# Kernel tuning notes

Hardware: AMD Instinct MI355X
Metric: run time of the kernel (lower is better)

The kernel has to match this reference:

```python
import jax, jax.numpy as jnp
import numpy as np

B, N, F, U, NH = 1, 4096, 32, 32, 2
NEG = -1e10


def _leaky(x):
    # tf.nn.leaky_relu default alpha = 0.2
    return jnp.where(x >= 0, x, 0.2 * x)


def setup_inputs() -> dict:
    key = jax.random.key(0)
    k = jax.random.split(key, 6)
    H_r = jax.random.normal(k[0], (B, N, F), dtype=jnp.float32)
    H_i = jax.random.normal(k[1], (B, N, F), dtype=jnp.float32)
    # sparse-ish adjacency with self loops, stored dense as the module expects
    adj = (jax.random.uniform(k[2], (B, N, N)) < 0.005).astype(jnp.float32)
    A = jnp.maximum(adj, jnp.eye(N, dtype=jnp.float32)[None])
    s_w = float(np.sqrt(6.0 / (F + U)))
    s_a = float(np.sqrt(6.0 / (U + 1)))
    W = jax.random.uniform(k[3], (NH, F, U), minval=-s_w, maxval=s_w, dtype=jnp.float32)
    a1 = jax.random.uniform(k[4], (NH, U), minval=-s_a, maxval=s_a, dtype=jnp.float32)
    a2 = jax.random.uniform(k[5], (NH, U), minval=-s_a, maxval=s_a, dtype=jnp.float32)
    return {"H_r": H_r, "H_i": H_i, "A": A, "W": W, "a1": a1, "a2": a2}


def reference(H_r, H_i, A, W, a1, a2):
    # complex X = H @ W  (W real): decompose into real/imag, vectorized over heads
    Xr = jnp.einsum('bnf,hfu->hbnu', H_r, W)   # [NH,B,N,U]
    Xi = jnp.einsum('bnf,hfu->hbnu', H_i, W)
    # additive attention logits: self + neighbours^T
    sr = jnp.einsum('hbnu,hu->hbn', Xr, a1)
    si = jnp.einsum('hbnu,hu->hbn', Xi, a1)
    nr = jnp.einsum('hbnu,hu->hbn', Xr, a2)
    ni = jnp.einsum('hbnu,hu->hbn', Xi, a2)
    E1 = _leaky(sr[..., :, None] + nr[..., None, :])   # [NH,B,N,N]
    E2 = _leaky(si[..., :, None] + ni[..., None, :])
    mask = NEG * (1.0 - A)                              # [B,N,N], broadcasts over heads
    alpha1 = jax.nn.softmax(E1 + mask, axis=-1)
    alpha2 = jax.nn.softmax(E2 + mask, axis=-1)
    # complex alpha @ complex X
    Hr_cap = jnp.einsum('hbij,hbju->hbiu', alpha1, Xr) - jnp.einsum('hbij,hbju->hbiu', alpha2, Xi)
    Hi_cap = jnp.einsum('hbij,hbju->hbiu', alpha1, Xi) + jnp.einsum('hbij,hbju->hbiu', alpha2, Xr)
    # concat heads on feature dim (output_layer=False, activation=identity)
    out_r = jnp.transpose(Hr_cap, (1, 2, 0, 3)).reshape(B, N, NH * U)
    out_i = jnp.transpose(Hi_cap, (1, 2, 0, 3)).reshape(B, N, NH * U)
    return (out_r, out_i)
```

## Files before the change

### kernel.cpp

```cpp
#include <hip/hip_runtime.h>
#include <math.h>

namespace {
constexpr int N  = 4096;
constexpr int F  = 32;
constexpr int U  = 32;
constexpr int NH = 2;
constexpr int MAXNBR = 1024;

__device__ __forceinline__ float leaky(float x) {
    return x >= 0.f ? x : 0.2f * x;
}

__device__ __forceinline__ float wred_max(float v) {
    #pragma unroll
    for (int m = 32; m; m >>= 1) v = fmaxf(v, __shfl_xor(v, m, 64));
    return v;
}
__device__ __forceinline__ float wred_sum(float v) {
    #pragma unroll
    for (int m = 32; m; m >>= 1) v += __shfl_xor(v, m, 64);
    return v;
}

__global__ __launch_bounds__(256) void proj_kernel(
    const float* __restrict__ Hr, const float* __restrict__ Hi,
    const float* __restrict__ W,  const float* __restrict__ a1,
    const float* __restrict__ a2,
    float* __restrict__ Xr, float* __restrict__ Xi,
    float* __restrict__ sr, float* __restrict__ si,
    float* __restrict__ nr, float* __restrict__ ni)
{
    __shared__ float sW[NH * F * U];
    __shared__ float sH[2][8][F];
    const int t = threadIdx.x;
    for (int k = t; k < NH * F * U; k += 256) sW[k] = W[k];
    const int row0 = blockIdx.x * 8;
    {
        const int r = t >> 5, f = t & 31;
        sH[0][r][f] = Hr[(row0 + r) * F + f];
        sH[1][r][f] = Hi[(row0 + r) * F + f];
    }
    __syncthreads();

    const int r = t >> 5, u = t & 31;
    const int n = row0 + r;
    float xr[NH] = {0.f, 0.f}, xi[NH] = {0.f, 0.f};
    #pragma unroll
    for (int h = 0; h < NH; ++h) {
        #pragma unroll
        for (int f = 0; f < F; ++f) {
            const float w = sW[h * F * U + f * U + u];
            xr[h] += sH[0][r][f] * w;
            xi[h] += sH[1][r][f] * w;
        }
    }
    #pragma unroll
    for (int h = 0; h < NH; ++h) {
        Xr[(h * N + n) * U + u] = xr[h];
        Xi[(h * N + n) * U + u] = xi[h];
    }
    #pragma unroll
    for (int h = 0; h < NH; ++h) {
        const float av1 = a1[h * U + u], av2 = a2[h * U + u];
        float vsr = xr[h] * av1, vnr = xr[h] * av2;
        float vsi = xi[h] * av1, vni = xi[h] * av2;
        #pragma unroll
        for (int m = 16; m; m >>= 1) {
            vsr += __shfl_xor(vsr, m, 32);
            vnr += __shfl_xor(vnr, m, 32);
            vsi += __shfl_xor(vsi, m, 32);
            vni += __shfl_xor(vni, m, 32);
        }
        if (u == 0) {
            sr[h * N + n] = vsr;
            nr[h * N + n] = vnr;
            si[h * N + n] = vsi;
            ni[h * N + n] = vni;
        }
    }
}

__global__ __launch_bounds__(256) void attn_kernel(
    const float* __restrict__ A,
    const float* __restrict__ Xr, const float* __restrict__ Xi,
    const float* __restrict__ sr, const float* __restrict__ si,
    const float* __restrict__ nr, const float* __restrict__ ni,
    float* __restrict__ out)
{
    __shared__ int   s_nbr[MAXNBR];
    __shared__ float s_e[4][MAXNBR];
    __shared__ float s_pmax[4][4];
    __shared__ float s_psum[4][4];
    __shared__ float s_accr[256];
    __shared__ float s_acci[256];
    __shared__ int   s_cnt;

    const int i = blockIdx.x;
    const int t = threadIdx.x;
    const int lane = t & 63, wv = t >> 6;

    if (t == 0) s_cnt = 0;
    __syncthreads();

    const float4* Arow = (const float4*)(A + (size_t)i * N);
    #pragma unroll
    for (int k = t; k < N / 4; k += 256) {
        const float4 v = Arow[k];
        if (v.x != 0.f) { int p = atomicAdd(&s_cnt, 1); if (p < MAXNBR) s_nbr[p] = 4 * k + 0; }
        if (v.y != 0.f) { int p = atomicAdd(&s_cnt, 1); if (p < MAXNBR) s_nbr[p] = 4 * k + 1; }
        if (v.z != 0.f) { int p = atomicAdd(&s_cnt, 1); if (p < MAXNBR) s_nbr[p] = 4 * k + 2; }
        if (v.w != 0.f) { int p = atomicAdd(&s_cnt, 1); if (p < MAXNBR) s_nbr[p] = 4 * k + 3; }
    }
    __syncthreads();
    const int cnt = min(s_cnt, MAXNBR);

    float sri[NH], sii[NH];
    #pragma unroll
    for (int h = 0; h < NH; ++h) { sri[h] = sr[h * N + i]; sii[h] = si[h * N + i]; }

    float m[4] = {-INFINITY, -INFINITY, -INFINITY, -INFINITY};
    for (int j = t; j < cnt; j += 256) {
        const int nj = s_nbr[j];
        #pragma unroll
        for (int h = 0; h < NH; ++h) {
            const float e1 = leaky(sri[h] + nr[h * N + nj]);
            const float e2 = leaky(sii[h] + ni[h * N + nj]);
            s_e[2 * h + 0][j] = e1;
            s_e[2 * h + 1][j] = e2;
            m[2 * h + 0] = fmaxf(m[2 * h + 0], e1);
            m[2 * h + 1] = fmaxf(m[2 * h + 1], e2);
        }
    }
    #pragma unroll
    for (int v = 0; v < 4; ++v) {
        const float wm = wred_max(m[v]);
        if (lane == 0) s_pmax[wv][v] = wm;
    }
    __syncthreads();
    float mx[4], sum[4];
    #pragma unroll
    for (int v = 0; v < 4; ++v) {
        mx[v] = fmaxf(fmaxf(s_pmax[0][v], s_pmax[1][v]),
                      fmaxf(s_pmax[2][v], s_pmax[3][v]));
        sum[v] = 0.f;
    }

    for (int j = t; j < cnt; j += 256) {
        #pragma unroll
        for (int v = 0; v < 4; ++v) {
            const float w = __expf(s_e[v][j] - mx[v]);
            s_e[v][j] = w;
            sum[v] += w;
        }
    }
    #pragma unroll
    for (int v = 0; v < 4; ++v) {
        const float ws = wred_sum(sum[v]);
        if (lane == 0) s_psum[wv][v] = ws;
    }
    __syncthreads();
    float rinv[4];
    #pragma unroll
    for (int v = 0; v < 4; ++v)
        rinv[v] = 1.f / (s_psum[0][v] + s_psum[1][v] + s_psum[2][v] + s_psum[3][v]);

    const int g = t >> 6, h = (t >> 5) & 1, u = t & 31;
    const float r1 = rinv[2 * h + 0], r2 = rinv[2 * h + 1];
    float accr = 0.f, acci = 0.f;
    for (int j = g; j < cnt; j += 4) {
        const int nj = s_nbr[j];
        const float w1 = s_e[2 * h + 0][j] * r1;
        const float w2 = s_e[2 * h + 1][j] * r2;
        const float xr = Xr[(h * N + nj) * U + u];
        const float xi = Xi[(h * N + nj) * U + u];
        accr += w1 * xr - w2 * xi;
        acci += w1 * xi + w2 * xr;
    }
    s_accr[t] = accr;
    s_acci[t] = acci;
    __syncthreads();
    if (g == 0) {
        const float vr = s_accr[t] + s_accr[t + 64] + s_accr[t + 128] + s_accr[t + 192];
        const float vi = s_acci[t] + s_acci[t + 64] + s_acci[t + 128] + s_acci[t + 192];
        out[(size_t)i * (NH * U) + h * U + u] = vr;
        out[(size_t)N * NH * U + (size_t)i * (NH * U) + h * U + u] = vi;
    }
}
}

extern "C" void kernel_launch(void* const* d_in, const int* in_sizes, int n_in,
                              void* d_out, int out_size, void* d_ws, size_t ws_size,
                              hipStream_t stream) {
    (void)in_sizes; (void)n_in; (void)out_size; (void)ws_size;
    const float* Hr = (const float*)d_in[0];
    const float* Hi = (const float*)d_in[1];
    const float* A  = (const float*)d_in[2];
    const float* W  = (const float*)d_in[3];
    const float* a1 = (const float*)d_in[4];
    const float* a2 = (const float*)d_in[5];
    float* out = (float*)d_out;

    float* ws = (float*)d_ws;
    float* Xr = ws;
    float* Xi = Xr + NH * N * U;
    float* sr = Xi + NH * N * U;
    float* si = sr + NH * N;
    float* nr = si + NH * N;
    float* ni = nr + NH * N;

    proj_kernel<<<N / 8, 256, 0, stream>>>(Hr, Hi, W, a1, a2, Xr, Xi, sr, si, nr, ni);
    attn_kernel<<<N, 256, 0, stream>>>(A, Xr, Xi, sr, si, nr, ni, out);
}
```

Baseline: 120.5 us.

## Use one wave per row with ballot scan and online softmax

The attention kernel now gives each row to a single wavefront instead of a 256-thread block. Neighbours are found with wave ballots over the adjacency row (with a one-step prefetch) rather than shared-memory atomics. Softmax and aggregation are fused into a single online-softmax pass, and real/imag projections are interleaved as float2 so each neighbour needs one load. This removes the block barriers, shared buffers and the neighbour cap, at the cost of extra exp calls per neighbour and a serial per-neighbour dependency chain inside each wave.

```diff
diff --git a/kernel.cpp b/kernel.cpp
--- a/kernel.cpp
+++ b/kernel.cpp
@@ -6,30 +6,16 @@
 constexpr int F  = 32;
 constexpr int U  = 32;
 constexpr int NH = 2;
-constexpr int MAXNBR = 1024;
 
 __device__ __forceinline__ float leaky(float x) {
     return x >= 0.f ? x : 0.2f * x;
-}
-
-__device__ __forceinline__ float wred_max(float v) {
-    #pragma unroll
-    for (int m = 32; m; m >>= 1) v = fmaxf(v, __shfl_xor(v, m, 64));
-    return v;
-}
-__device__ __forceinline__ float wred_sum(float v) {
-    #pragma unroll
-    for (int m = 32; m; m >>= 1) v += __shfl_xor(v, m, 64);
-    return v;
 }
 
 __global__ __launch_bounds__(256) void proj_kernel(
     const float* __restrict__ Hr, const float* __restrict__ Hi,
     const float* __restrict__ W,  const float* __restrict__ a1,
     const float* __restrict__ a2,
-    float* __restrict__ Xr, float* __restrict__ Xi,
-    float* __restrict__ sr, float* __restrict__ si,
-    float* __restrict__ nr, float* __restrict__ ni)
+    float2* __restrict__ Xp, float2* __restrict__ Sp, float2* __restrict__ Np)
 {
     __shared__ float sW[NH * F * U];
     __shared__ float sH[2][8][F];
@@ -56,10 +42,9 @@
         }
     }
     #pragma unroll
-    for (int h = 0; h < NH; ++h) {
-        Xr[(h * N + n) * U + u] = xr[h];
-        Xi[(h * N + n) * U + u] = xi[h];
-    }
+    for (int h = 0; h < NH; ++h)
+        Xp[(h * N + n) * U + u] = make_float2(xr[h], xi[h]);
+
     #pragma unroll
     for (int h = 0; h < NH; ++h) {
         const float av1 = a1[h * U + u], av2 = a2[h * U + u];
@@ -73,119 +58,70 @@
             vni += __shfl_xor(vni, m, 32);
         }
         if (u == 0) {
-            sr[h * N + n] = vsr;
-            nr[h * N + n] = vnr;
-            si[h * N + n] = vsi;
-            ni[h * N + n] = vni;
+            Sp[h * N + n] = make_float2(vsr, vsi);
+            Np[h * N + n] = make_float2(vnr, vni);
         }
     }
 }
 
 __global__ __launch_bounds__(256) void attn_kernel(
     const float* __restrict__ A,
-    const float* __restrict__ Xr, const float* __restrict__ Xi,
-    const float* __restrict__ sr, const float* __restrict__ si,
-    const float* __restrict__ nr, const float* __restrict__ ni,
+    const float2* __restrict__ Xp, const float2* __restrict__ Sp,
+    const float2* __restrict__ Np,
     float* __restrict__ out)
 {
-    __shared__ int   s_nbr[MAXNBR];
-    __shared__ float s_e[4][MAXNBR];
-    __shared__ float s_pmax[4][4];
-    __shared__ float s_psum[4][4];
-    __shared__ float s_accr[256];
-    __shared__ float s_acci[256];
-    __shared__ int   s_cnt;
+    const int wv   = threadIdx.x >> 6;
+    const int lane = threadIdx.x & 63;
+    const int i    = blockIdx.x * 4 + wv;
+    const int h    = lane >> 5;
 
-    const int i = blockIdx.x;
-    const int t = threadIdx.x;
-    const int lane = t & 63, wv = t >> 6;
+    const float2 s = Sp[h * N + i];
 
-    if (t == 0) s_cnt = 0;
-    __syncthreads();
+    float m1 = -INFINITY, m2 = -INFINITY;
+    float l1 = 0.f, l2 = 0.f;
+    float a1r = 0.f, a1i = 0.f, a2r = 0.f, a2i = 0.f;
 
-    const float4* Arow = (const float4*)(A + (size_t)i * N);
-    #pragma unroll
-    for (int k = t; k < N / 4; k += 256) {
-        const float4 v = Arow[k];
-        if (v.x != 0.f) { int p = atomicAdd(&s_cnt, 1); if (p < MAXNBR) s_nbr[p] = 4 * k + 0; }
-        if (v.y != 0.f) { int p = atomicAdd(&s_cnt, 1); if (p < MAXNBR) s_nbr[p] = 4 * k + 1; }
-        if (v.z != 0.f) { int p = atomicAdd(&s_cnt, 1); if (p < MAXNBR) s_nbr[p] = 4 * k + 2; }
-        if (v.w != 0.f) { int p = atomicAdd(&s_cnt, 1); if (p < MAXNBR) s_nbr[p] = 4 * k + 3; }
+    const float4* __restrict__ Arow = (const float4*)(A + (size_t)i * N);
+    float4 v = Arow[lane];
+    #pragma unroll 1
+    for (int c = 0; c < N / 256; ++c) {
+        float4 vn;
+        if (c < N / 256 - 1) vn = Arow[(c + 1) * 64 + lane];
+        unsigned long long mk0 = __ballot(v.x != 0.f);
+        unsigned long long mk1 = __ballot(v.y != 0.f);
+        unsigned long long mk2 = __ballot(v.z != 0.f);
+        unsigned long long mk3 = __ballot(v.w != 0.f);
+        #pragma unroll
+        for (int cc = 0; cc < 4; ++cc) {
+            unsigned long long mask = (cc == 0) ? mk0 : (cc == 1) ? mk1
+                                    : (cc == 2) ? mk2 : mk3;
+            while (mask) {
+                const int b = __ffsll((unsigned long long)mask) - 1;
+                mask &= mask - 1;
+                const int nj = c * 256 + 4 * b + cc;
+                const float2 nn = Np[h * N + nj];
+                const float e1 = leaky(s.x + nn.x);
+                const float e2 = leaky(s.y + nn.y);
+                const float m1n = fmaxf(m1, e1), m2n = fmaxf(m2, e2);
+                const float c1 = __expf(m1 - m1n);
+                const float c2 = __expf(m2 - m2n);
+                const float w1 = __expf(e1 - m1n);
+                const float w2 = __expf(e2 - m2n);
+                m1 = m1n; m2 = m2n;
+                l1 = l1 * c1 + w1;
+                l2 = l2 * c2 + w2;
+                const float2 x = Xp[(h * N + nj) * U + (lane & 31)];
+                a1r = a1r * c1 + w1 * x.x;
+                a1i = a1i * c1 + w1 * x.y;
+                a2r = a2r * c2 + w2 * x.x;
+                a2i = a2i * c2 + w2 * x.y;
+            }
+        }
+        v = vn;
     }
-    __syncthreads();
-    const int cnt = min(s_cnt, MAXNBR);
-
-    float sri[NH], sii[NH];
-    #pragma unroll
-    for (int h = 0; h < NH; ++h) { sri[h] = sr[h * N + i]; sii[h] = si[h * N + i]; }
-
-    float m[4] = {-INFINITY, -INFINITY, -INFINITY, -INFINITY};
-    for (int j = t; j < cnt; j += 256) {
-        const int nj = s_nbr[j];
-        #pragma unroll
-        for (int h = 0; h < NH; ++h) {
-            const float e1 = leaky(sri[h] + nr[h * N + nj]);
-            const float e2 = leaky(sii[h] + ni[h * N + nj]);
-            s_e[2 * h + 0][j] = e1;
-            s_e[2 * h + 1][j] = e2;
-            m[2 * h + 0] = fmaxf(m[2 * h + 0], e1);
-            m[2 * h + 1] = fmaxf(m[2 * h + 1], e2);
-        }
-    }
-    #pragma unroll
-    for (int v = 0; v < 4; ++v) {
-        const float wm = wred_max(m[v]);
-        if (lane == 0) s_pmax[wv][v] = wm;
-    }
-    __syncthreads();
-    float mx[4], sum[4];
-    #pragma unroll
-    for (int v = 0; v < 4; ++v) {
-        mx[v] = fmaxf(fmaxf(s_pmax[0][v], s_pmax[1][v]),
-                      fmaxf(s_pmax[2][v], s_pmax[3][v]));
-        sum[v] = 0.f;
-    }
-
-    for (int j = t; j < cnt; j += 256) {
-        #pragma unroll
-        for (int v = 0; v < 4; ++v) {
-            const float w = __expf(s_e[v][j] - mx[v]);
-            s_e[v][j] = w;
-            sum[v] += w;
-        }
-    }
-    #pragma unroll
-    for (int v = 0; v < 4; ++v) {
-        const float ws = wred_sum(sum[v]);
-        if (lane == 0) s_psum[wv][v] = ws;
-    }
-    __syncthreads();
-    float rinv[4];
-    #pragma unroll
-    for (int v = 0; v < 4; ++v)
-        rinv[v] = 1.f / (s_psum[0][v] + s_psum[1][v] + s_psum[2][v] + s_psum[3][v]);
-
-    const int g = t >> 6, h = (t >> 5) & 1, u = t & 31;
-    const float r1 = rinv[2 * h + 0], r2 = rinv[2 * h + 1];
-    float accr = 0.f, acci = 0.f;
-    for (int j = g; j < cnt; j += 4) {
-        const int nj = s_nbr[j];
-        const float w1 = s_e[2 * h + 0][j] * r1;
-        const float w2 = s_e[2 * h + 1][j] * r2;
-        const float xr = Xr[(h * N + nj) * U + u];
-        const float xi = Xi[(h * N + nj) * U + u];
-        accr += w1 * xr - w2 * xi;
-        acci += w1 * xi + w2 * xr;
-    }
-    s_accr[t] = accr;
-    s_acci[t] = acci;
-    __syncthreads();
-    if (g == 0) {
-        const float vr = s_accr[t] + s_accr[t + 64] + s_accr[t + 128] + s_accr[t + 192];
-        const float vi = s_acci[t] + s_acci[t + 64] + s_acci[t + 128] + s_acci[t + 192];
-        out[(size_t)i * (NH * U) + h * U + u] = vr;
-        out[(size_t)N * NH * U + (size_t)i * (NH * U) + h * U + u] = vi;
-    }
+    const float r1 = 1.f / l1, r2 = 1.f / l2;
+    out[(size_t)i * (NH * U) + lane]                     = a1r * r1 - a2i * r2;
+    out[(size_t)N * NH * U + (size_t)i * (NH * U) + lane] = a1i * r1 + a2r * r2;
 }
 }
 
@@ -201,14 +137,11 @@
     const float* a2 = (const float*)d_in[5];
     float* out = (float*)d_out;
 
-    float* ws = (float*)d_ws;
-    float* Xr = ws;
-    float* Xi = Xr + NH * N * U;
-    float* sr = Xi + NH * N * U;
-    float* si = sr + NH * N;
-    float* nr = si + NH * N;
-    float* ni = nr + NH * N;
+    float2* ws = (float2*)d_ws;
+    float2* Xp = ws;
+    float2* Sp = Xp + NH * N * U;
+    float2* Np = Sp + NH * N;
 
-    proj_kernel<<<N / 8, 256, 0, stream>>>(Hr, Hi, W, a1, a2, Xr, Xi, sr, si, nr, ni);
-    attn_kernel<<<N, 256, 0, stream>>>(A, Xr, Xi, sr, si, nr, ni, out);
+    proj_kernel<<<N / 8, 256, 0, stream>>>(Hr, Hi, W, a1, a2, Xp, Sp, Np);
+    attn_kernel<<<N / 4, 256, 0, stream>>>(A, Xp, Sp, Np, out);
 }
```

Result: slower. 123.8 us (+2.8%).
